# Optimization experiments

Hardware: AMD Instinct MI355X
Metric: run time of the kernel (lower is better)

## Reference

```python
import jax, jax.numpy as jnp
from jax import lax
import numpy as np

# Constants from the source module
DMIN, DMAX = 1.0, 50.0
NUM_PLANES = 8            # number of depth-hypothesis planes
FOCAL = 307.98 // 4.0     # focal // downsample (stride-4 features) -> 76.0 px

B, C, H, W = 4, 64, 96, 320


def _plane_shifts(dtype):
    # reciprocal (inverse-depth) spaced hypothesis planes: d_i = 1/disp_i
    disp = jnp.linspace(1.0 / DMAX, 1.0 / DMIN, NUM_PLANES, dtype=dtype)
    return (FOCAL * disp).astype(dtype)  # per-plane vertical pixel shift f/d


def _warp_vertical(x, shifts):
    """Bilinear vertical homography warp of x [B,C,H,W] for each shift.
    Returns [B,D,C,H,W]; out-of-image samples are zero."""
    Bb, Cc, Hh, Ww = x.shape
    D = shifts.shape[0]
    y = jnp.arange(Hh, dtype=x.dtype)                 # [H]
    y_src = y[None, :] + shifts[:, None]              # [D,H]
    y0 = jnp.floor(y_src)
    w = (y_src - y0)                                  # bilinear weight [D,H]
    y0i = y0.astype(jnp.int32)
    y1i = y0i + 1
    v0 = ((y0i >= 0) & (y0i < Hh)).astype(x.dtype)    # validity masks [D,H]
    v1 = ((y1i >= 0) & (y1i < Hh)).astype(x.dtype)
    y0c = jnp.clip(y0i, 0, Hh - 1).reshape(-1)        # [D*H]
    y1c = jnp.clip(y1i, 0, Hh - 1).reshape(-1)
    # gather rows: [B,C,D*H,W] -> [B,C,D,H,W]
    g0 = jnp.take(x, y0c, axis=2).reshape(Bb, Cc, D, Hh, Ww)
    g1 = jnp.take(x, y1c, axis=2).reshape(Bb, Cc, D, Hh, Ww)
    wb = w[None, None, :, :, None]
    out = (1.0 - wb) * v0[None, None, :, :, None] * g0 + wb * v1[None, None, :, :, None] * g1
    return jnp.transpose(out, (0, 2, 1, 3, 4))        # [B,D,C,H,W]


def _depth_recip_conv(x, Wk, b):
    """Warp to each hypothesis plane, conv each, max-project over planes."""
    Bb, Cc, Hh, Ww = x.shape
    warped = _warp_vertical(x, _plane_shifts(x.dtype))        # [B,D,C,H,W]
    D = warped.shape[1]
    xr = warped.reshape(Bb * D, Cc, Hh, Ww)
    y = lax.conv_general_dilated(xr, Wk, window_strides=(1, 1), padding='SAME',
                                 dimension_numbers=('NCHW', 'OIHW', 'NCHW'))
    Co = Wk.shape[0]
    y = y.reshape(Bb, D, Co, Hh, Ww).max(axis=1)              # max-projection
    return y + b[None, :, None, None]


def setup_inputs() -> dict:
    key = jax.random.key(0)
    k1, k2, k3, k4, k5 = jax.random.split(key, 5)
    fan = C * 9
    return {
        'x': jax.random.normal(k1, (B, C, H, W), dtype=jnp.float32),
        'W1': jax.random.normal(k2, (C, C, 3, 3), dtype=jnp.float32) / np.sqrt(fan),
        'b1': jax.random.normal(k3, (C,), dtype=jnp.float32) * 0.01,
        'W2': jax.random.normal(k4, (C, C, 3, 3), dtype=jnp.float32) / np.sqrt(fan),
        'b2': jax.random.normal(k5, (C,), dtype=jnp.float32) * 0.01,
    }


def reference(x, W1, b1, W2, b2):
    x = jax.nn.relu(_depth_recip_conv(x, W1, b1))
    x = jax.nn.relu(_depth_recip_conv(x, W2, b2))
    return x
```

## Files before the change

kernel.cpp:

```cpp
#include <hip/hip_runtime.h>
#include <math.h>

#define HH 96
#define WW 320
#define NP 8

typedef _Float16 half8_t  __attribute__((ext_vector_type(8)));
typedef _Float16 half4_t  __attribute__((ext_vector_type(4)));
typedef float    floatx16 __attribute__((ext_vector_type(16)));

struct ShiftInfo {
    int   s0[NP];
    float wa[NP];
    float wb[NP];
    int   rows[16];
};

__device__ __forceinline__ void gl_lds16(const _Float16* g, _Float16* l) {
    __builtin_amdgcn_global_load_lds(
        (const __attribute__((address_space(1))) void*)g,
        (__attribute__((address_space(3))) void*)l, 16, 0, 0);
}

__global__ __launch_bounds__(256) void prep_kernel(
    const float* __restrict__ X, const float* __restrict__ W1,
    const float* __restrict__ W2, _Float16* __restrict__ Xt,
    _Float16* __restrict__ Wf)
{
    __shared__ __align__(16) _Float16 Ls[64 * 163];
    const int bx = blockIdx.x, t = threadIdx.x;
    if (bx < 768) {
        const int r = bx >> 1, xh = bx & 1;
        const int y = r % HH, b = r / HH;
        const int xbase = xh * 160;
        for (int u = t; u < 64 * 40; u += 256) {
            int ci = u / 40;
            int xi = (u - ci * 40) * 4;
            float4 v = *(const float4*)&X[((size_t)(b * 64 + ci) * HH + y) * WW + xbase + xi];
            half4_t hv = { (_Float16)v.x, (_Float16)v.y, (_Float16)v.z, (_Float16)v.w };
            *(half4_t*)&Ls[ci * 163 + xi] = hv;
        }
        __syncthreads();
        const int ci8 = t & 7, xg = t >> 3;
        for (int it = 0; it < 5; ++it) {
            int x = xg + 32 * it;
            half8_t o;
#pragma unroll
            for (int j = 0; j < 8; ++j) o[j] = Ls[(ci8 * 8 + j) * 163 + x];
            *(half8_t*)&Xt[((size_t)(b * HH + y) * WW + xbase + x) * 64 + ci8 * 8] = o;
        }
    } else {
        const int k = bx - 768;
        const int layer = k / 9, pos = k - layer * 9;
        const float* Ws = layer ? W2 : W1;
        _Float16* Wd = Wf + layer * 36864 + pos * 4096;
        for (int u = t; u < 4096; u += 256) {
            int mt  = u >> 11;
            int ks  = (u >> 9) & 3;
            int i31 = (u >> 4) & 31;
            int h   = (u >> 3) & 1;
            int j   = u & 7;
            int co  = mt * 32 + i31;
            int ci  = ks * 16 + h * 8 + j;
            Wd[u] = (_Float16)Ws[((size_t)co * 64 + ci) * 9 + pos];
        }
    }
}

template<int MODE, int NPOS>
__device__ __forceinline__ void conv_core(
    const _Float16* __restrict__ Xs, int w, int i31, int h,
    const _Float16* wp0, floatx16 (&acc)[2][2])
{
    constexpr int NI = NPOS * 4;
    half8_t fw0[4], fw1[4], fx0[4], fx1[4];

    int xsw[3], xbase[3];
#pragma unroll
    for (int kx = 0; kx < 3; ++kx) {
        int x = i31 + kx;
        xsw[kx]   = x & 7;
        xbase[kx] = x * 64;
    }
    const int rowb = w * (66 * 64);

    auto ld = [&](int idx, int s) {
        const int pos = idx >> 2, ks = idx & 3;
        const int ky = pos / 3, kx = pos - ky * 3;
        const _Float16* wp = wp0 + pos * 4096 + ks * 512;
        fw0[s] = *(const half8_t*)(wp);
        fw1[s] = *(const half8_t*)(wp + 2048);
        const int c8  = ks * 2 + h;
        const int off = rowb + ky * (66 * 64) + xbase[kx] + ((c8 ^ xsw[kx]) * 8);
        fx0[s] = *(const half8_t*)(Xs + off);
        fx1[s] = *(const half8_t*)(Xs + off + 32 * 64);
    };

#pragma unroll
    for (int s = 0; s < 3; ++s) ld(s, s);

#pragma unroll
    for (int i = 0; i < NI; ++i) {
        if (i + 3 < NI) ld(i + 3, (i + 3) & 3);
        const int s = i & 3;
        if (MODE == 1) {
            acc[0][0] = __builtin_amdgcn_mfma_f32_32x32x16_f16(fx0[s], fw0[s], acc[0][0], 0, 0, 0);
            acc[0][1] = __builtin_amdgcn_mfma_f32_32x32x16_f16(fx0[s], fw1[s], acc[0][1], 0, 0, 0);
            acc[1][0] = __builtin_amdgcn_mfma_f32_32x32x16_f16(fx1[s], fw0[s], acc[1][0], 0, 0, 0);
            acc[1][1] = __builtin_amdgcn_mfma_f32_32x32x16_f16(fx1[s], fw1[s], acc[1][1], 0, 0, 0);
        } else {
            acc[0][0] = __builtin_amdgcn_mfma_f32_32x32x16_f16(fw0[s], fx0[s], acc[0][0], 0, 0, 0);
            acc[0][1] = __builtin_amdgcn_mfma_f32_32x32x16_f16(fw0[s], fx1[s], acc[0][1], 0, 0, 0);
            acc[1][0] = __builtin_amdgcn_mfma_f32_32x32x16_f16(fw1[s], fx0[s], acc[1][0], 0, 0, 0);
            acc[1][1] = __builtin_amdgcn_mfma_f32_32x32x16_f16(fw1[s], fx1[s], acc[1][1], 0, 0, 0);
        }
    }
}

template<int MODE>
__global__ __launch_bounds__(256, 3) void conv_kernel(
    const _Float16* __restrict__ Xt, const _Float16* __restrict__ Wfl,
    _Float16* __restrict__ OutE, _Float16* __restrict__ OutT, ShiftInfo si)
{
    __shared__ __align__(16) _Float16 Xs[6 * 66 * 64];
    const int xt = blockIdx.x, rg = blockIdx.y, b = blockIdx.z;
    const bool top = rg >= 24;
    const int trg = rg - 24;
    const int x0 = xt * 64;
    const int t  = threadIdx.x;

    int grow[6];
#pragma unroll
    for (int r = 0; r < 6; ++r)
        grow[r] = top ? ((r < 4) ? si.rows[trg * 4 + r] : -1) : rg * 4 + r;

#pragma unroll
    for (int r = 0; r < 6; ++r) {
        if ((unsigned)grow[r] >= HH) {
            for (int u = t; u < 66 * 8; u += 256) {
                float4 zz = make_float4(0.f, 0.f, 0.f, 0.f);
                *(float4*)&Xs[r * (66 * 64) + u * 8] = zz;
            }
        }
    }

    if (t < 96) {
        int r  = t >> 4, hx = (t >> 3) & 1, c8 = t & 7;
        int x  = hx ? 65 : 0;
        int gx = x0 - 1 + x;
        float4 v = make_float4(0.f, 0.f, 0.f, 0.f);
        if ((unsigned)grow[r] < HH && (unsigned)gx < WW)
            v = *(const float4*)&Xt[((size_t)(b * HH + grow[r]) * WW + gx) * 64 + c8 * 8];
        *(float4*)&Xs[(r * 66 + x) * 64 + ((c8 ^ (x & 7)) * 8)] = v;
    }

    {
        const int w = t >> 6, l = t & 63;
#pragma unroll
        for (int j = 0; j < 12; ++j) {
            int k = w + 4 * j;
            int r = k >> 3, c = k & 7;
            if ((unsigned)grow[r] < HH) {
                int x  = 1 + 8 * c + (l >> 3);
                int c8 = (l & 7) ^ (x & 7);
                const _Float16* g =
                    &Xt[((size_t)(b * HH + grow[r]) * WW + (x0 - 1 + x)) * 64 + c8 * 8];
                gl_lds16(g, &Xs[(r * 66 + 1 + 8 * c) * 64]);
            }
        }
    }
    __syncthreads();

    const int l = t & 63, w = t >> 6;
    const int i31 = l & 31, h = l >> 5;

    floatx16 acc[2][2];
#pragma unroll
    for (int a = 0; a < 2; ++a)
#pragma unroll
        for (int c = 0; c < 2; ++c)
            acc[a][c] = (floatx16){0.f,0.f,0.f,0.f, 0.f,0.f,0.f,0.f,
                                   0.f,0.f,0.f,0.f, 0.f,0.f,0.f,0.f};

    const _Float16* wp0 = Wfl + i31 * 16 + h * 8;
    if (top) conv_core<MODE, 3>(Xs, w, i31, h, wp0, acc);
    else     conv_core<MODE, 9>(Xs, w, i31, h, wp0, acc);

    const int OH = top ? 16 : HH;
    const int om = top ? (trg * 4 + w) : (rg * 4 + w);
    _Float16* Out = top ? OutT : OutE;
#pragma unroll
    for (int a = 0; a < 2; ++a)
#pragma unroll
        for (int c = 0; c < 2; ++c)
#pragma unroll
            for (int r = 0; r < 16; ++r) {
                int dm = (r & 3) + 8 * (r >> 2) + 4 * h;
                if (MODE == 1) {
                    int x  = x0 + a * 32 + dm;
                    int co = c * 32 + i31;
                    Out[((size_t)(b * OH + om) * WW + x) * 64 + co] = (_Float16)acc[a][c][r];
                } else {
                    int co = a * 32 + dm;
                    int x  = x0 + c * 32 + i31;
                    Out[((size_t)(b * 64 + co) * OH + om) * WW + x] = (_Float16)acc[a][c][r];
                }
            }
}

__global__ __launch_bounds__(256) void blend1_kernel(
    const _Float16* __restrict__ Cb, const _Float16* __restrict__ T,
    const float* __restrict__ bias, _Float16* __restrict__ Xt2, ShiftInfo si)
{
    __shared__ __align__(16) _Float16 Cs[96 * 2 * 64];
    __shared__ __align__(16) _Float16 Ts[16 * 2 * 64];
    const int xt = blockIdx.x, b = blockIdx.y, t = threadIdx.x;
    const int x0 = xt * 2;
    const half8_t z = {0,0,0,0,0,0,0,0};

    {
        const int w = t >> 6, l = t & 63;
        const int v = l & 15;
#pragma unroll
        for (int j = 0; j < 6; ++j) {
            int k = w + 4 * j;
            int row = 4 * k + (l >> 4);
            gl_lds16(&Cb[((size_t)(b * HH + row) * WW + x0 + (v >> 3)) * 64 + (v & 7) * 8],
                     &Cs[k * 512]);
        }
        {
            int k = w;
            int row = 4 * k + (l >> 4);
            gl_lds16(&T[((size_t)(b * 16 + row) * WW + x0 + (v >> 3)) * 64 + (v & 7) * 8],
                     &Ts[k * 512]);
        }
    }
    __syncthreads();

    const int co8 = t & 7, xl = (t >> 3) & 1, yt = t >> 4;
    half8_t bv;
#pragma unroll
    for (int j = 0; j < 8; ++j) bv[j] = (_Float16)bias[co8 * 8 + j];

    const int y0 = yt * 6;
    half8_t cur[NP];
#pragma unroll
    for (int d = 0; d < NP; ++d) {
        int r = y0 + si.s0[d] - 1;
        cur[d] = (r < HH) ? *(const half8_t*)&Cs[((r * 2 + xl) * 64) + co8 * 8] : z;
    }
    for (int y = y0; y < y0 + 6; ++y) {
        half8_t m = z;
#pragma unroll
        for (int d = 0; d < NP; ++d) {
            int r1 = y + si.s0[d];
            half8_t v1 = (r1 < HH) ? *(const half8_t*)&Cs[((r1 * 2 + xl) * 64) + co8 * 8] : z;
            half8_t v0 = cur[d];
            cur[d] = v1;
            _Float16 a = (_Float16)si.wa[d], wg = (_Float16)si.wb[d];
            half8_t p;
            if (y == 0) {
                half8_t t0 = *(const half8_t*)&Ts[(((2 * d) * 2 + xl) * 64) + co8 * 8];
                half8_t t1 = *(const half8_t*)&Ts[(((2 * d + 1) * 2 + xl) * 64) + co8 * 8];
                p = a * (v0 - t0) + wg * (v1 - t1);
            } else {
                p = a * v0 + wg * v1;
            }
            m = (d == 0) ? p : __builtin_elementwise_max(m, p);
        }
        half8_t o = __builtin_elementwise_max(m + bv, z);
        *(half8_t*)&Xt2[((size_t)(b * HH + y) * WW + x0 + xl) * 64 + co8 * 8] = o;
    }
}

__global__ __launch_bounds__(256) void blend2_kernel(
    const _Float16* __restrict__ Cb, const _Float16* __restrict__ T,
    const float* __restrict__ bias, float* __restrict__ Out, ShiftInfo si)
{
    __shared__ __align__(16) _Float16 Cs[96 * 64];
    __shared__ __align__(16) _Float16 Ts[16 * 64];
    const int task = blockIdx.x, t = threadIdx.x;
    const int xt = task % 5;
    const int rem = task / 5;
    const int co = rem & 63;
    const int b  = rem >> 6;
    const int x0 = xt * 64;
    const half8_t z = {0,0,0,0,0,0,0,0};

    {
        const int w = t >> 6, l = t & 63;
        const int x8 = l & 7;
#pragma unroll
        for (int j = 0; j < 3; ++j) {
            int k = w + 4 * j;
            int row = 8 * k + (l >> 3);
            gl_lds16(&Cb[((size_t)(b * 64 + co) * HH + row) * WW + x0 + x8 * 8],
                     &Cs[k * 512]);
        }
        if (w < 2) {
            int k = w;
            int row = 8 * k + (l >> 3);
            gl_lds16(&T[((size_t)(b * 64 + co) * 16 + row) * WW + x0 + x8 * 8],
                     &Ts[k * 512]);
        }
    }
    __syncthreads();

    const int x8 = t & 7, yt = t >> 3;
    const float bvf = bias[co];
    const int y0 = yt * 3;

    half8_t cur[NP];
#pragma unroll
    for (int d = 0; d < NP; ++d) {
        int r = y0 + si.s0[d] - 1;
        cur[d] = (r < HH) ? *(const half8_t*)&Cs[r * 64 + x8 * 8] : z;
    }
    for (int y = y0; y < y0 + 3; ++y) {
        half8_t m = z;
#pragma unroll
        for (int d = 0; d < NP; ++d) {
            int r1 = y + si.s0[d];
            half8_t v1 = (r1 < HH) ? *(const half8_t*)&Cs[r1 * 64 + x8 * 8] : z;
            half8_t v0 = cur[d];
            cur[d] = v1;
            _Float16 a = (_Float16)si.wa[d], wg = (_Float16)si.wb[d];
            half8_t p;
            if (y == 0) {
                half8_t t0 = *(const half8_t*)&Ts[(2 * d) * 64 + x8 * 8];
                half8_t t1 = *(const half8_t*)&Ts[(2 * d + 1) * 64 + x8 * 8];
                p = a * (v0 - t0) + wg * (v1 - t1);
            } else {
                p = a * v0 + wg * v1;
            }
            m = (d == 0) ? p : __builtin_elementwise_max(m, p);
        }
        float4 o0, o1;
        o0.x = fmaxf((float)m[0] + bvf, 0.f);
        o0.y = fmaxf((float)m[1] + bvf, 0.f);
        o0.z = fmaxf((float)m[2] + bvf, 0.f);
        o0.w = fmaxf((float)m[3] + bvf, 0.f);
        o1.x = fmaxf((float)m[4] + bvf, 0.f);
        o1.y = fmaxf((float)m[5] + bvf, 0.f);
        o1.z = fmaxf((float)m[6] + bvf, 0.f);
        o1.w = fmaxf((float)m[7] + bvf, 0.f);
        float* op = Out + ((size_t)(b * 64 + co) * HH + y) * WW + x0 + x8 * 8;
        *(float4*)op = o0;
        *(float4*)(op + 4) = o1;
    }
}

extern "C" void kernel_launch(void* const* d_in, const int* in_sizes, int n_in,
                              void* d_out, int out_size, void* d_ws, size_t ws_size,
                              hipStream_t stream) {
    const float* x  = (const float*)d_in[0];
    const float* W1 = (const float*)d_in[1];
    const float* b1 = (const float*)d_in[2];
    const float* W2 = (const float*)d_in[3];
    const float* b2 = (const float*)d_in[4];
    float* out = (float*)d_out;

    _Float16* Xt1 = (_Float16*)d_ws;
    _Float16* Cb  = Xt1 + 7864320;
    _Float16* T   = Cb  + 7864320;
    _Float16* Wf  = T   + 1310720;
    _Float16* Xt2 = (_Float16*)d_out;

    ShiftInfo si;
    for (int d = 0; d < NP; ++d) {
        double disp = 0.02 + d * (0.98 / 7.0);
        double sh   = 76.0 * disp;
        int s0      = (int)floor(sh);
        double w    = sh - (double)s0;
        si.s0[d] = s0;
        si.wa[d] = (float)(1.0 - w);
        si.wb[d] = (float)w;
        si.rows[2 * d]     = s0 - 1;
        si.rows[2 * d + 1] = s0;
    }

    prep_kernel<<<dim3(786), 256, 0, stream>>>(x, W1, W2, Xt1, Wf);

    conv_kernel<1><<<dim3(5, 28, 4), 256, 0, stream>>>(Xt1, Wf, Cb, T, si);
    blend1_kernel<<<dim3(160, 4), 256, 0, stream>>>(Cb, T, b1, Xt2, si);

    conv_kernel<2><<<dim3(5, 28, 4), 256, 0, stream>>>(Xt2, Wf + 36864, Cb, T, si);
    blend2_kernel<<<dim3(1280), 256, 0, stream>>>(Cb, T, b2, out, si);
}
```

Before: 79.87 us.

## Deepen weight prefetch, issue async LDS loads first, halve blend1 block tile

The conv inner loop now prefetches weight fragments five steps ahead in a six-slot ring, kept separate from the activation fragments, which still use a three-ahead, four-slot ring. In the conv prologue the async global-to-LDS loads are issued before the zero-fill and halo stores, so those stores overlap the in-flight copies. blend1 now handles one x column per block instead of two, doubling the grid and halving shared memory per block to raise parallelism. The extra weight registers may lower occupancy for the 3-blocks-per-CU conv kernel.

```diff
diff --git a/kernel.cpp b/kernel.cpp
--- a/kernel.cpp
+++ b/kernel.cpp
@@ -73,7 +73,7 @@
     const _Float16* wp0, floatx16 (&acc)[2][2])
 {
     constexpr int NI = NPOS * 4;
-    half8_t fw0[4], fw1[4], fx0[4], fx1[4];
+    half8_t fw0[6], fw1[6], fx0[4], fx1[4];
 
     int xsw[3], xbase[3];
 #pragma unroll
@@ -84,12 +84,15 @@
     }
     const int rowb = w * (66 * 64);
 
-    auto ld = [&](int idx, int s) {
+    auto ldw = [&](int idx, int s) {
         const int pos = idx >> 2, ks = idx & 3;
-        const int ky = pos / 3, kx = pos - ky * 3;
         const _Float16* wp = wp0 + pos * 4096 + ks * 512;
         fw0[s] = *(const half8_t*)(wp);
         fw1[s] = *(const half8_t*)(wp + 2048);
+    };
+    auto ldx = [&](int idx, int s) {
+        const int pos = idx >> 2, ks = idx & 3;
+        const int ky = pos / 3, kx = pos - ky * 3;
         const int c8  = ks * 2 + h;
         const int off = rowb + ky * (66 * 64) + xbase[kx] + ((c8 ^ xsw[kx]) * 8);
         fx0[s] = *(const half8_t*)(Xs + off);
@@ -97,22 +100,25 @@
     };
 
 #pragma unroll
-    for (int s = 0; s < 3; ++s) ld(s, s);
+    for (int s = 0; s < 5; ++s) ldw(s, s);
+#pragma unroll
+    for (int s = 0; s < 3; ++s) ldx(s, s);
 
 #pragma unroll
     for (int i = 0; i < NI; ++i) {
-        if (i + 3 < NI) ld(i + 3, (i + 3) & 3);
-        const int s = i & 3;
+        if (i + 5 < NI) ldw(i + 5, (i + 5) % 6);
+        if (i + 3 < NI) ldx(i + 3, (i + 3) & 3);
+        const int sw = i % 6, sx = i & 3;
         if (MODE == 1) {
-            acc[0][0] = __builtin_amdgcn_mfma_f32_32x32x16_f16(fx0[s], fw0[s], acc[0][0], 0, 0, 0);
-            acc[0][1] = __builtin_amdgcn_mfma_f32_32x32x16_f16(fx0[s], fw1[s], acc[0][1], 0, 0, 0);
-            acc[1][0] = __builtin_amdgcn_mfma_f32_32x32x16_f16(fx1[s], fw0[s], acc[1][0], 0, 0, 0);
-            acc[1][1] = __builtin_amdgcn_mfma_f32_32x32x16_f16(fx1[s], fw1[s], acc[1][1], 0, 0, 0);
+            acc[0][0] = __builtin_amdgcn_mfma_f32_32x32x16_f16(fx0[sx], fw0[sw], acc[0][0], 0, 0, 0);
+            acc[0][1] = __builtin_amdgcn_mfma_f32_32x32x16_f16(fx0[sx], fw1[sw], acc[0][1], 0, 0, 0);
+            acc[1][0] = __builtin_amdgcn_mfma_f32_32x32x16_f16(fx1[sx], fw0[sw], acc[1][0], 0, 0, 0);
+            acc[1][1] = __builtin_amdgcn_mfma_f32_32x32x16_f16(fx1[sx], fw1[sw], acc[1][1], 0, 0, 0);
         } else {
-            acc[0][0] = __builtin_amdgcn_mfma_f32_32x32x16_f16(fw0[s], fx0[s], acc[0][0], 0, 0, 0);
-            acc[0][1] = __builtin_amdgcn_mfma_f32_32x32x16_f16(fw0[s], fx1[s], acc[0][1], 0, 0, 0);
-            acc[1][0] = __builtin_amdgcn_mfma_f32_32x32x16_f16(fw1[s], fx0[s], acc[1][0], 0, 0, 0);
-            acc[1][1] = __builtin_amdgcn_mfma_f32_32x32x16_f16(fw1[s], fx1[s], acc[1][1], 0, 0, 0);
+            acc[0][0] = __builtin_amdgcn_mfma_f32_32x32x16_f16(fw0[sw], fx0[sx], acc[0][0], 0, 0, 0);
+            acc[0][1] = __builtin_amdgcn_mfma_f32_32x32x16_f16(fw0[sw], fx1[sx], acc[0][1], 0, 0, 0);
+            acc[1][0] = __builtin_amdgcn_mfma_f32_32x32x16_f16(fw1[sw], fx0[sx], acc[1][0], 0, 0, 0);
+            acc[1][1] = __builtin_amdgcn_mfma_f32_32x32x16_f16(fw1[sw], fx1[sx], acc[1][1], 0, 0, 0);
         }
     }
 }
@@ -133,26 +139,6 @@
 #pragma unroll
     for (int r = 0; r < 6; ++r)
         grow[r] = top ? ((r < 4) ? si.rows[trg * 4 + r] : -1) : rg * 4 + r;
-
-#pragma unroll
-    for (int r = 0; r < 6; ++r) {
-        if ((unsigned)grow[r] >= HH) {
-            for (int u = t; u < 66 * 8; u += 256) {
-                float4 zz = make_float4(0.f, 0.f, 0.f, 0.f);
-                *(float4*)&Xs[r * (66 * 64) + u * 8] = zz;
-            }
-        }
-    }
-
-    if (t < 96) {
-        int r  = t >> 4, hx = (t >> 3) & 1, c8 = t & 7;
-        int x  = hx ? 65 : 0;
-        int gx = x0 - 1 + x;
-        float4 v = make_float4(0.f, 0.f, 0.f, 0.f);
-        if ((unsigned)grow[r] < HH && (unsigned)gx < WW)
-            v = *(const float4*)&Xt[((size_t)(b * HH + grow[r]) * WW + gx) * 64 + c8 * 8];
-        *(float4*)&Xs[(r * 66 + x) * 64 + ((c8 ^ (x & 7)) * 8)] = v;
-    }
 
     {
         const int w = t >> 6, l = t & 63;
@@ -168,6 +154,26 @@
                 gl_lds16(g, &Xs[(r * 66 + 1 + 8 * c) * 64]);
             }
         }
+    }
+
+#pragma unroll
+    for (int r = 0; r < 6; ++r) {
+        if ((unsigned)grow[r] >= HH) {
+            for (int u = t; u < 66 * 8; u += 256) {
+                float4 zz = make_float4(0.f, 0.f, 0.f, 0.f);
+                *(float4*)&Xs[r * (66 * 64) + u * 8] = zz;
+            }
+        }
+    }
+
+    if (t < 96) {
+        int r  = t >> 4, hx = (t >> 3) & 1, c8 = t & 7;
+        int x  = hx ? 65 : 0;
+        int gx = x0 - 1 + x;
+        float4 v = make_float4(0.f, 0.f, 0.f, 0.f);
+        if ((unsigned)grow[r] < HH && (unsigned)gx < WW)
+            v = *(const float4*)&Xt[((size_t)(b * HH + grow[r]) * WW + gx) * 64 + c8 * 8];
+        *(float4*)&Xs[(r * 66 + x) * 64 + ((c8 ^ (x & 7)) * 8)] = v;
     }
     __syncthreads();
 
@@ -212,56 +218,54 @@
     const _Float16* __restrict__ Cb, const _Float16* __restrict__ T,
     const float* __restrict__ bias, _Float16* __restrict__ Xt2, ShiftInfo si)
 {
-    __shared__ __align__(16) _Float16 Cs[96 * 2 * 64];
-    __shared__ __align__(16) _Float16 Ts[16 * 2 * 64];
-    const int xt = blockIdx.x, b = blockIdx.y, t = threadIdx.x;
-    const int x0 = xt * 2;
+    __shared__ __align__(16) _Float16 Cs[96 * 64];
+    __shared__ __align__(16) _Float16 Ts[16 * 64];
+    const int x0 = blockIdx.x, b = blockIdx.y, t = threadIdx.x;
     const half8_t z = {0,0,0,0,0,0,0,0};
 
     {
         const int w = t >> 6, l = t & 63;
-        const int v = l & 15;
-#pragma unroll
-        for (int j = 0; j < 6; ++j) {
+        const int c8 = l & 7;
+#pragma unroll
+        for (int j = 0; j < 3; ++j) {
             int k = w + 4 * j;
-            int row = 4 * k + (l >> 4);
-            gl_lds16(&Cb[((size_t)(b * HH + row) * WW + x0 + (v >> 3)) * 64 + (v & 7) * 8],
+            int row = 8 * k + (l >> 3);
+            gl_lds16(&Cb[((size_t)(b * HH + row) * WW + x0) * 64 + c8 * 8],
                      &Cs[k * 512]);
         }
-        {
-            int k = w;
-            int row = 4 * k + (l >> 4);
-            gl_lds16(&T[((size_t)(b * 16 + row) * WW + x0 + (v >> 3)) * 64 + (v & 7) * 8],
-                     &Ts[k * 512]);
+        if (w < 2) {
+            int row = 8 * w + (l >> 3);
+            gl_lds16(&T[((size_t)(b * 16 + row) * WW + x0) * 64 + c8 * 8],
+                     &Ts[w * 512]);
         }
     }
     __syncthreads();
 
-    const int co8 = t & 7, xl = (t >> 3) & 1, yt = t >> 4;
+    const int co8 = t & 7, yt = t >> 3;
     half8_t bv;
 #pragma unroll
     for (int j = 0; j < 8; ++j) bv[j] = (_Float16)bias[co8 * 8 + j];
 
-    const int y0 = yt * 6;
+    const int y0 = yt * 3;
     half8_t cur[NP];
 #pragma unroll
     for (int d = 0; d < NP; ++d) {
         int r = y0 + si.s0[d] - 1;
-        cur[d] = (r < HH) ? *(const half8_t*)&Cs[((r * 2 + xl) * 64) + co8 * 8] : z;
-    }
-    for (int y = y0; y < y0 + 6; ++y) {
+        cur[d] = (r < HH) ? *(const half8_t*)&Cs[r * 64 + co8 * 8] : z;
+    }
+    for (int y = y0; y < y0 + 3; ++y) {
         half8_t m = z;
 #pragma unroll
         for (int d = 0; d < NP; ++d) {
             int r1 = y + si.s0[d];
-            half8_t v1 = (r1 < HH) ? *(const half8_t*)&Cs[((r1 * 2 + xl) * 64) + co8 * 8] : z;
+            half8_t v1 = (r1 < HH) ? *(const half8_t*)&Cs[r1 * 64 + co8 * 8] : z;
             half8_t v0 = cur[d];
             cur[d] = v1;
             _Float16 a = (_Float16)si.wa[d], wg = (_Float16)si.wb[d];
             half8_t p;
             if (y == 0) {
-                half8_t t0 = *(const half8_t*)&Ts[(((2 * d) * 2 + xl) * 64) + co8 * 8];
-                half8_t t1 = *(const half8_t*)&Ts[(((2 * d + 1) * 2 + xl) * 64) + co8 * 8];
+                half8_t t0 = *(const half8_t*)&Ts[(2 * d) * 64 + co8 * 8];
+                half8_t t1 = *(const half8_t*)&Ts[(2 * d + 1) * 64 + co8 * 8];
                 p = a * (v0 - t0) + wg * (v1 - t1);
             } else {
                 p = a * v0 + wg * v1;
@@ -269,7 +273,7 @@
             m = (d == 0) ? p : __builtin_elementwise_max(m, p);
         }
         half8_t o = __builtin_elementwise_max(m + bv, z);
-        *(half8_t*)&Xt2[((size_t)(b * HH + y) * WW + x0 + xl) * 64 + co8 * 8] = o;
+        *(half8_t*)&Xt2[((size_t)(b * HH + y) * WW + x0) * 64 + co8 * 8] = o;
     }
 }
 
@@ -298,10 +302,9 @@
                      &Cs[k * 512]);
         }
         if (w < 2) {
-            int k = w;
-            int row = 8 * k + (l >> 3);
+            int row = 8 * w + (l >> 3);
             gl_lds16(&T[((size_t)(b * 64 + co) * 16 + row) * WW + x0 + x8 * 8],
-                     &Ts[k * 512]);
+                     &Ts[w * 512]);
         }
     }
     __syncthreads();
@@ -382,7 +385,7 @@
     prep_kernel<<<dim3(786), 256, 0, stream>>>(x, W1, W2, Xt1, Wf);
 
     conv_kernel<1><<<dim3(5, 28, 4), 256, 0, stream>>>(Xt1, Wf, Cb, T, si);
-    blend1_kernel<<<dim3(160, 4), 256, 0, stream>>>(Cb, T, b1, Xt2, si);
+    blend1_kernel<<<dim3(320, 4), 256, 0, stream>>>(Cb, T, b1, Xt2, si);
 
     conv_kernel<2><<<dim3(5, 28, 4), 256, 0, stream>>>(Xt2, Wf + 36864, Cb, T, si);
     blend2_kernel<<<dim3(1280), 256, 0, stream>>>(Cb, T, b2, out, si);
```

Result: slower. 84.20 us (+5.4%).
